# Optimization experiments

Hardware: AMD Instinct MI355X
Metric: run time of the kernel (lower is better)

## Reference

```python
import jax, jax.numpy as jnp
import numpy as np

EMBED_DIM = 128
NUM_HEADS = 4
HEAD_DIM = EMBED_DIM // NUM_HEADS


def setup_inputs() -> dict:
    key = jax.random.key(0)
    ks = jax.random.split(key, 12)
    B, N, D = 4, 4096, EMBED_DIM
    s = 1.0 / np.sqrt(D)
    inp = {
        "query": jax.random.normal(ks[0], (B, N, D), dtype=jnp.float32),
        "key": jax.random.normal(ks[1], (B, N, D), dtype=jnp.float32),
        "value": jax.random.normal(ks[2], (B, N, D), dtype=jnp.float32),
        "Wq": jax.random.uniform(ks[3], (D, D), jnp.float32, -s, s),
        "bq": jax.random.uniform(ks[4], (D,), jnp.float32, -s, s),
        "Wk": jax.random.uniform(ks[5], (D, D), jnp.float32, -s, s),
        "bk": jax.random.uniform(ks[6], (D,), jnp.float32, -s, s),
        "Wv": jax.random.uniform(ks[7], (D, D), jnp.float32, -s, s),
        "bv": jax.random.uniform(ks[8], (D,), jnp.float32, -s, s),
        "Wo": jax.random.uniform(ks[9], (D, D), jnp.float32, -s, s),
        "bo": jax.random.uniform(ks[10], (D,), jnp.float32, -s, s),
    }
    return inp


def reference(query, key, value, Wq, bq, Wk, bk, Wv, bv, Wo, bo):
    B, N, D = query.shape
    H, Dh = NUM_HEADS, HEAD_DIM
    scale = Dh ** -0.5
    # Linear projections (torch Linear: x @ W.T + b), split heads -> [B, H, N, Dh]
    Q = (query @ Wq.T + bq).reshape(B, N, H, Dh).transpose(0, 2, 1, 3)
    K = (key @ Wk.T + bk).reshape(B, N, H, Dh).transpose(0, 2, 1, 3)
    V = (value @ Wv.T + bv).reshape(B, N, H, Dh).transpose(0, 2, 1, 3)
    # Attention scores [B, H, N, N]
    scores = jnp.einsum('bhqd,bhkd->bhqk', Q, K) * scale
    attn = jax.nn.softmax(scores, axis=-1)
    ctx = jnp.einsum('bhqk,bhkd->bhqd', attn, V)  # [B, H, N, Dh]
    ctx = ctx.transpose(0, 2, 1, 3).reshape(B, N, D)
    return ctx @ Wo.T + bo
```

## Files before the change

### kernel.cpp

```cpp
#include <hip/hip_runtime.h>
#include <hip/hip_bf16.h>

#define N_SEQ 4096
#define DIM   128
#define NH    4
#define DH    32
#define BATCH 4

#define QSCALE 0.25503495870989204f

typedef __bf16 bf16x8 __attribute__((ext_vector_type(8)));
typedef __bf16 bf16x2 __attribute__((ext_vector_type(2)));
typedef __bf16 bf16x4 __attribute__((ext_vector_type(4)));
typedef float  f32x4  __attribute__((ext_vector_type(4)));

#define MFMA(a, b, c) __builtin_amdgcn_mfma_f32_16x16x32_bf16((a), (b), (c), 0, 0, 0)

static __device__ __forceinline__ bf16x8 cvt8(const float* __restrict__ p) {
    const float4* f4 = reinterpret_cast<const float4*>(p);
    float4 a = f4[0], b = f4[1];
    bf16x8 r;
    r[0] = (__bf16)a.x; r[1] = (__bf16)a.y; r[2] = (__bf16)a.z; r[3] = (__bf16)a.w;
    r[4] = (__bf16)b.x; r[5] = (__bf16)b.y; r[6] = (__bf16)b.z; r[7] = (__bf16)b.w;
    return r;
}

static __device__ __forceinline__ f32x4 exp4(f32x4 s) {
    f32x4 r;
    r[0] = __builtin_amdgcn_exp2f(s[0]);
    r[1] = __builtin_amdgcn_exp2f(s[1]);
    r[2] = __builtin_amdgcn_exp2f(s[2]);
    r[3] = __builtin_amdgcn_exp2f(s[3]);
    return r;
}

static __device__ __forceinline__ bf16x8 pack8(f32x4 a, f32x4 b) {
    bf16x8 o;
    o[0] = (__bf16)a[0]; o[1] = (__bf16)a[1];
    o[2] = (__bf16)a[2]; o[3] = (__bf16)a[3];
    o[4] = (__bf16)b[0]; o[5] = (__bf16)b[1];
    o[6] = (__bf16)b[2]; o[7] = (__bf16)b[3];
    return o;
}

__global__ __launch_bounds__(256) void proj_qkv(
    const float* __restrict__ xq, const float* __restrict__ xk, const float* __restrict__ xv,
    const float* __restrict__ Wq, const float* __restrict__ Wk, const float* __restrict__ Wv,
    const float* __restrict__ bq, const float* __restrict__ bk, const float* __restrict__ bv,
    __bf16* __restrict__ Qs, __bf16* __restrict__ Kb, __bf16* __restrict__ Vt)
{
    __shared__ __align__(16) char wlds[34816];
    const int z = blockIdx.z;
    const float* x    = (z == 0) ? xq : ((z == 1) ? xk : xv);
    const float* Wf   = (z == 0) ? Wq : ((z == 1) ? Wk : Wv);
    const float* bias = (z == 0) ? bq : ((z == 1) ? bk : bv);
    const int b    = blockIdx.y;
    const int tid  = threadIdx.x;
    const int wave = tid >> 6, lane = tid & 63;
    const int quad = lane >> 4, l15 = lane & 15;
    const int n0   = blockIdx.x * 64 + wave * 16;

    {
        const int r = tid >> 1, half = tid & 1;
        const float* wsrc = Wf + r * DIM + half * 64;
        char* wdst = wlds + r * 272 + half * 128;
        #pragma unroll
        for (int i = 0; i < 8; i++)
            *(bf16x8*)(wdst + i * 16) = cvt8(wsrc + i * 8);
    }

    bf16x8 a[4];
    const float* xrow = x + (b * N_SEQ + n0 + l15) * DIM + quad * 8;
    a[0] = cvt8(xrow);      a[1] = cvt8(xrow + 32);
    a[2] = cvt8(xrow + 64); a[3] = cvt8(xrow + 96);
    __syncthreads();

    const int n = n0 + l15;
    for (int t = 0; t < 8; t++) {
        const char* wr = wlds + (t * 16 + l15) * 272 + quad * 16;
        bf16x8 w0 = *(const bf16x8*)(wr);
        bf16x8 w1 = *(const bf16x8*)(wr + 64);
        bf16x8 w2 = *(const bf16x8*)(wr + 128);
        bf16x8 w3 = *(const bf16x8*)(wr + 192);

        f32x4 acc = {0.f, 0.f, 0.f, 0.f};
        acc = MFMA(w0, a[0], acc);
        acc = MFMA(w1, a[1], acc);
        acc = MFMA(w2, a[2], acc);
        acc = MFMA(w3, a[3], acc);

        const int d0 = t * 16 + quad * 4;
        if (z == 0) {
            const int h = d0 >> 5, dh0 = d0 & 31;
            bf16x4 q4;
            #pragma unroll
            for (int r = 0; r < 4; r++)
                q4[r] = (__bf16)((acc[r] + bias[d0 + r]) * QSCALE);
            *(bf16x4*)(Qs + ((b * NH + h) * N_SEQ + n) * DH + dh0) = q4;
        } else if (z == 1) {
            const int h = d0 >> 5, dh0 = d0 & 31;
            bf16x4 k4;
            #pragma unroll
            for (int r = 0; r < 4; r++)
                k4[r] = (__bf16)(acc[r] + bias[d0 + r]);
            *(bf16x4*)(Kb + ((b * NH + h) * N_SEQ + n) * DH + dh0) = k4;
        } else {
            const int nl = n & 63;
            const int np = (n & ~63) | (nl & 35) | ((nl & 12) << 1) | ((nl & 16) >> 2);
            #pragma unroll
            for (int r = 0; r < 4; r++) {
                const int d = d0 + r, h = d >> 5, dh = d & 31;
                Vt[((b * NH + h) * DH + dh) * N_SEQ + np] = (__bf16)(acc[r] + bias[d]);
            }
        }
    }
}

__global__ __launch_bounds__(256, 2) void flash_attn(
    const __bf16* __restrict__ Qs, const __bf16* __restrict__ Kb,
    const __bf16* __restrict__ Vt, __bf16* __restrict__ ctxb)
{
    __shared__ __align__(16) char smem[77824];
    char* const Kbase = smem;
    char* const Vbase = smem + 40960;

    const int bid  = blockIdx.x;
    const int bh   = bid & 15;
    const int qc   = bid >> 4;
    const int tid  = threadIdx.x;
    const int wave = tid >> 6, lane = tid & 63;
    const int quad = lane >> 4, l15 = lane & 15;
    const int qh   = wave & 1, kh = wave >> 1;
    const int n0   = qc * 128 + qh * 64;
    const int KH   = 2048;

    const __bf16* Qp = Qs + (bh * N_SEQ + n0) * DH;
    bf16x8 qf[4];
    #pragma unroll
    for (int q = 0; q < 4; q++)
        qf[q] = *(const bf16x8*)(Qp + (q * 16 + l15) * DH + quad * 8);

    bf16x8 ones;
    #pragma unroll
    for (int i = 0; i < 8; i++) ones[i] = (__bf16)1.0f;

    const int r_ = tid >> 2, c_ = tid & 3;
    const __bf16* gK = Kb + (size_t)bh * N_SEQ * DH + r_ * DH + c_ * 8;
    const __bf16* gV = Vt + ((size_t)bh * DH + (tid >> 3)) * N_SEQ + (tid & 7) * 8;
    const int kofsK = r_ * 80 + c_ * 16;
    const int kofsV = (tid >> 3) * 144 + (tid & 7) * 16;

    {
        #pragma unroll
        for (int g = 0; g < 2; g++) {
            #pragma unroll
            for (int t = 0; t < 2; t++) {
                bf16x8 kr = *(const bf16x8*)(gK + (size_t)(g * KH + t * 64) * DH);
                bf16x8 vr = *(const bf16x8*)(gV + g * KH + t * 64);
                *(bf16x8*)(Kbase + g * 20480 + t * 5120 + kofsK) = kr;
                *(bf16x8*)(Vbase + g * 18432 + t * 4608 + kofsV) = vr;
            }
        }
    }
    __syncthreads();

    char* const Kme = Kbase + kh * 20480;
    char* const Vme = Vbase + kh * 18432;

    f32x4 c[4][2];
    f32x4 cl[4];
    const f32x4 z4 = {0.f,0.f,0.f,0.f};
    #pragma unroll
    for (int q = 0; q < 4; q++) { c[q][0] = z4; c[q][1] = z4; cl[q] = z4; }

    for (int kbb = 0; kbb < KH / 128; kbb++) {
        const int cur = kbb & 1;
        const char* Kc = Kme + cur * 10240;
        const char* Vc = Vme + cur * 9216;

        const int kn = (kbb + 1) & (KH / 128 - 1);
        bf16x8 krn[2][2], vrn[2][2];
        #pragma unroll
        for (int g = 0; g < 2; g++) {
            #pragma unroll
            for (int t = 0; t < 2; t++) {
                krn[g][t] = *(const bf16x8*)(gK + (size_t)(g * KH + kn * 128 + t * 64) * DH);
                vrn[g][t] = *(const bf16x8*)(gV + g * KH + kn * 128 + t * 64);
            }
        }

        bf16x8 kfa[2][4], vfa[2][4];
        #pragma unroll
        for (int t = 0; t < 2; t++) {
            const char* Kt  = Kc + t * 5120;
            const char* Vtl = Vc + t * 4608;
            #pragma unroll
            for (int i = 0; i < 4; i++)
                kfa[t][i] = *(const bf16x8*)(Kt + (i * 16 + l15) * 80 + quad * 16);
            vfa[t][0] = *(const bf16x8*)(Vtl + l15 * 144 + quad * 16);
            vfa[t][1] = *(const bf16x8*)(Vtl + (16 + l15) * 144 + quad * 16);
            vfa[t][2] = *(const bf16x8*)(Vtl + l15 * 144 + 64 + quad * 16);
            vfa[t][3] = *(const bf16x8*)(Vtl + (16 + l15) * 144 + 64 + quad * 16);
        }

        #pragma unroll
        for (int t = 0; t < 2; t++) {
            bf16x8 pf[4][2];
            #pragma unroll
            for (int q = 0; q < 4; q++) {
                __builtin_amdgcn_s_setprio(1);
                f32x4 sa = MFMA(kfa[t][0], qf[q], z4);
                f32x4 sb = MFMA(kfa[t][1], qf[q], z4);
                f32x4 sc = MFMA(kfa[t][2], qf[q], z4);
                f32x4 sd = MFMA(kfa[t][3], qf[q], z4);
                __builtin_amdgcn_s_setprio(0);
                f32x4 ea = exp4(sa), eb = exp4(sb), ec = exp4(sc), ed = exp4(sd);
                pf[q][0] = pack8(ea, eb);
                pf[q][1] = pack8(ec, ed);
            }

            __builtin_amdgcn_s_setprio(1);
            #pragma unroll
            for (int q = 0; q < 4; q++) {
                c[q][0] = MFMA(vfa[t][0], pf[q][0], c[q][0]);
                c[q][1] = MFMA(vfa[t][1], pf[q][0], c[q][1]);
                c[q][0] = MFMA(vfa[t][2], pf[q][1], c[q][0]);
                c[q][1] = MFMA(vfa[t][3], pf[q][1], c[q][1]);
                cl[q]   = MFMA(ones, pf[q][0], cl[q]);
                cl[q]   = MFMA(ones, pf[q][1], cl[q]);
            }
            __builtin_amdgcn_s_setprio(0);
        }

        #pragma unroll
        for (int g = 0; g < 2; g++) {
            #pragma unroll
            for (int t = 0; t < 2; t++) {
                *(bf16x8*)(Kbase + g * 20480 + (cur ^ 1) * 10240 + t * 5120 + kofsK) = krn[g][t];
                *(bf16x8*)(Vbase + g * 18432 + (cur ^ 1) * 9216 + t * 4608 + kofsV) = vrn[g][t];
            }
        }
        __syncthreads();
    }


    if (kh == 1) {
        char* dst = smem + (qh * 64 + lane) * 144;
        #pragma unroll
        for (int q = 0; q < 4; q++) {
            *(f32x4*)(dst + (q * 2 + 0) * 16) = c[q][0];
            *(f32x4*)(dst + (q * 2 + 1) * 16) = c[q][1];
        }
        f32x4 lv = {cl[0][0], cl[1][0], cl[2][0], cl[3][0]};
        *(f32x4*)(dst + 128) = lv;
    }
    __syncthreads();
    if (kh == 0) {
        const char* src = smem + (qh * 64 + lane) * 144;
        f32x4 lp = *(const f32x4*)(src + 128);
        const int b = bh >> 2, h = bh & 3;
        #pragma unroll
        for (int q = 0; q < 4; q++) {
            c[q][0] += *(const f32x4*)(src + (q * 2 + 0) * 16);
            c[q][1] += *(const f32x4*)(src + (q * 2 + 1) * 16);
            const float inv = 1.0f / (cl[q][0] + lp[q]);
            const int qg = n0 + q * 16 + l15;
            __bf16* dst = ctxb + ((size_t)(b * N_SEQ + qg)) * DIM + h * DH + quad * 4;
            #pragma unroll
            for (int dt = 0; dt < 2; dt++) {
                f32x4 cc = c[q][dt];
                bf16x2 e0 = {(__bf16)(cc[0] * inv), (__bf16)(cc[1] * inv)};
                bf16x2 e1 = {(__bf16)(cc[2] * inv), (__bf16)(cc[3] * inv)};
                *(bf16x2*)(dst + dt * 16)     = e0;
                *(bf16x2*)(dst + dt * 16 + 2) = e1;
            }
        }
    }
}

__global__ __launch_bounds__(256) void out_proj(
    const __bf16* __restrict__ ctxb, const float* __restrict__ Wo,
    const float* __restrict__ bo, float* __restrict__ out)
{
    __shared__ __align__(16) char wlds[34816];
    const int b    = blockIdx.y;
    const int tid  = threadIdx.x;
    const int wave = tid >> 6, lane = tid & 63;
    const int quad = lane >> 4, l15 = lane & 15;
    const int n0   = blockIdx.x * 64 + wave * 16;

    {
        const int r = tid >> 1, half = tid & 1;
        const float* wsrc = Wo + r * DIM + half * 64;
        char* wdst = wlds + r * 272 + half * 128;
        #pragma unroll
        for (int i = 0; i < 8; i++)
            *(bf16x8*)(wdst + i * 16) = cvt8(wsrc + i * 8);
    }

    bf16x8 a[4];
    const __bf16* crow = ctxb + (b * N_SEQ + n0 + l15) * DIM + quad * 8;
    a[0] = *(const bf16x8*)(crow);
    a[1] = *(const bf16x8*)(crow + 32);
    a[2] = *(const bf16x8*)(crow + 64);
    a[3] = *(const bf16x8*)(crow + 96);
    __syncthreads();

    const int n = n0 + l15;
    for (int t = 0; t < 8; t++) {
        const char* wr = wlds + (t * 16 + l15) * 272 + quad * 16;
        bf16x8 w0 = *(const bf16x8*)(wr);
        bf16x8 w1 = *(const bf16x8*)(wr + 64);
        bf16x8 w2 = *(const bf16x8*)(wr + 128);
        bf16x8 w3 = *(const bf16x8*)(wr + 192);

        f32x4 acc = {0.f, 0.f, 0.f, 0.f};
        acc = MFMA(w0, a[0], acc);
        acc = MFMA(w1, a[1], acc);
        acc = MFMA(w2, a[2], acc);
        acc = MFMA(w3, a[3], acc);

        const int d0 = t * 16 + quad * 4;
        float4 o;
        o.x = acc[0] + bo[d0];
        o.y = acc[1] + bo[d0 + 1];
        o.z = acc[2] + bo[d0 + 2];
        o.w = acc[3] + bo[d0 + 3];
        *(float4*)(out + (b * N_SEQ + n) * DIM + d0) = o;
    }
}

extern "C" void kernel_launch(void* const* d_in, const int* in_sizes, int n_in,
                              void* d_out, int out_size, void* d_ws, size_t ws_size,
                              hipStream_t stream)
{
    const float* query = (const float*)d_in[0];
    const float* key   = (const float*)d_in[1];
    const float* value = (const float*)d_in[2];
    const float* Wq = (const float*)d_in[3];
    const float* bq = (const float*)d_in[4];
    const float* Wk = (const float*)d_in[5];
    const float* bk = (const float*)d_in[6];
    const float* Wv = (const float*)d_in[7];
    const float* bv = (const float*)d_in[8];
    const float* Wo = (const float*)d_in[9];
    const float* bo = (const float*)d_in[10];
    float* out = (float*)d_out;

    char* ws = (char*)d_ws;
    const size_t e = (size_t)BATCH * N_SEQ * DIM;
    __bf16* Qs   = (__bf16*)(ws);
    __bf16* Kb   = (__bf16*)(ws + 2 * e);
    __bf16* Vt   = (__bf16*)(ws + 4 * e);
    __bf16* ctxb = (__bf16*)(ws + 6 * e);

    proj_qkv<<<dim3(64, BATCH, 3), 256, 0, stream>>>(
        query, key, value, Wq, Wk, Wv, bq, bk, bv, Qs, Kb, Vt);
    flash_attn<<<dim3(512), 256, 0, stream>>>(Qs, Kb, Vt, ctxb);
    out_proj<<<dim3(64, BATCH), 256, 0, stream>>>(ctxb, Wo, bo, out);
}
```

Baseline: 147.4 us.

## Load K/V MFMA fragments directly from global into registers, dropping LDS staging

The flash attention loop no longer stages K and V tiles through double-buffered shared memory with a block-wide barrier each step. Each wave now loads its MFMA operand fragments straight from global memory into registers, using a two-register-set ping-pong prefetch. Shared memory shrinks to what the final cross-wave reduction needs. This removes LDS writes, LDS reads and __syncthreads per tile, which may allow higher occupancy. In exchange it gives up LDS reuse, so each wave issues its own strided global loads of K/V, which the L2 cache must absorb.

```diff
diff --git a/kernel.cpp b/kernel.cpp
--- a/kernel.cpp
+++ b/kernel.cpp
@@ -120,9 +120,7 @@
     const __bf16* __restrict__ Qs, const __bf16* __restrict__ Kb,
     const __bf16* __restrict__ Vt, __bf16* __restrict__ ctxb)
 {
-    __shared__ __align__(16) char smem[77824];
-    char* const Kbase = smem;
-    char* const Vbase = smem + 40960;
+    __shared__ __align__(16) char smem[18432];
 
     const int bid  = blockIdx.x;
     const int bh   = bid & 15;
@@ -144,28 +142,49 @@
     #pragma unroll
     for (int i = 0; i < 8; i++) ones[i] = (__bf16)1.0f;
 
-    const int r_ = tid >> 2, c_ = tid & 3;
-    const __bf16* gK = Kb + (size_t)bh * N_SEQ * DH + r_ * DH + c_ * 8;
-    const __bf16* gV = Vt + ((size_t)bh * DH + (tid >> 3)) * N_SEQ + (tid & 7) * 8;
-    const int kofsK = r_ * 80 + c_ * 16;
-    const int kofsV = (tid >> 3) * 144 + (tid & 7) * 16;
-
-    {
-        #pragma unroll
-        for (int g = 0; g < 2; g++) {
-            #pragma unroll
-            for (int t = 0; t < 2; t++) {
-                bf16x8 kr = *(const bf16x8*)(gK + (size_t)(g * KH + t * 64) * DH);
-                bf16x8 vr = *(const bf16x8*)(gV + g * KH + t * 64);
-                *(bf16x8*)(Kbase + g * 20480 + t * 5120 + kofsK) = kr;
-                *(bf16x8*)(Vbase + g * 18432 + t * 4608 + kofsV) = vr;
-            }
-        }
-    }
-    __syncthreads();
-
-    char* const Kme = Kbase + kh * 20480;
-    char* const Vme = Vbase + kh * 18432;
+    const __bf16* gK  = Kb + ((size_t)bh * N_SEQ + kh * KH + l15) * DH + quad * 8;
+    const __bf16* gV0 = Vt + ((size_t)bh * DH + l15) * N_SEQ + kh * KH + quad * 8;
+    const __bf16* gV1 = gV0 + 16 * N_SEQ;
+
+#define LOADT(t, k0,k1,k2,k3, v0,v1,v2,v3) do {                         \
+    const int _t = (t) & 31;                                            \
+    const __bf16* _k = gK + (size_t)(_t * 64) * DH;                     \
+    k0 = *(const bf16x8*)(_k);                                          \
+    k1 = *(const bf16x8*)(_k + 16 * DH);                                \
+    k2 = *(const bf16x8*)(_k + 32 * DH);                                \
+    k3 = *(const bf16x8*)(_k + 48 * DH);                                \
+    v0 = *(const bf16x8*)(gV0 + _t * 64);                               \
+    v1 = *(const bf16x8*)(gV1 + _t * 64);                               \
+    v2 = *(const bf16x8*)(gV0 + _t * 64 + 32);                          \
+    v3 = *(const bf16x8*)(gV1 + _t * 64 + 32);                          \
+} while (0)
+
+#define COMPUTE(k0,k1,k2,k3, v0,v1,v2,v3) do {                          \
+    bf16x8 pf[4][2];                                                    \
+    _Pragma("unroll")                                                   \
+    for (int q = 0; q < 4; q++) {                                       \
+        __builtin_amdgcn_s_setprio(1);                                  \
+        f32x4 sa = MFMA(k0, qf[q], z4);                                 \
+        f32x4 sb = MFMA(k1, qf[q], z4);                                 \
+        f32x4 sc = MFMA(k2, qf[q], z4);                                 \
+        f32x4 sd = MFMA(k3, qf[q], z4);                                 \
+        __builtin_amdgcn_s_setprio(0);                                  \
+        f32x4 ea = exp4(sa), eb = exp4(sb), ec = exp4(sc), ed = exp4(sd); \
+        pf[q][0] = pack8(ea, eb);                                       \
+        pf[q][1] = pack8(ec, ed);                                       \
+    }                                                                   \
+    __builtin_amdgcn_s_setprio(1);                                      \
+    _Pragma("unroll")                                                   \
+    for (int q = 0; q < 4; q++) {                                       \
+        c[q][0] = MFMA(v0, pf[q][0], c[q][0]);                          \
+        c[q][1] = MFMA(v1, pf[q][0], c[q][1]);                          \
+        c[q][0] = MFMA(v2, pf[q][1], c[q][0]);                          \
+        c[q][1] = MFMA(v3, pf[q][1], c[q][1]);                          \
+        cl[q]   = MFMA(ones, pf[q][0], cl[q]);                          \
+        cl[q]   = MFMA(ones, pf[q][1], cl[q]);                          \
+    }                                                                   \
+    __builtin_amdgcn_s_setprio(0);                                      \
+} while (0)
 
     f32x4 c[4][2];
     f32x4 cl[4];
@@ -173,76 +192,20 @@
     #pragma unroll
     for (int q = 0; q < 4; q++) { c[q][0] = z4; c[q][1] = z4; cl[q] = z4; }
 
-    for (int kbb = 0; kbb < KH / 128; kbb++) {
-        const int cur = kbb & 1;
-        const char* Kc = Kme + cur * 10240;
-        const char* Vc = Vme + cur * 9216;
-
-        const int kn = (kbb + 1) & (KH / 128 - 1);
-        bf16x8 krn[2][2], vrn[2][2];
-        #pragma unroll
-        for (int g = 0; g < 2; g++) {
-            #pragma unroll
-            for (int t = 0; t < 2; t++) {
-                krn[g][t] = *(const bf16x8*)(gK + (size_t)(g * KH + kn * 128 + t * 64) * DH);
-                vrn[g][t] = *(const bf16x8*)(gV + g * KH + kn * 128 + t * 64);
-            }
-        }
-
-        bf16x8 kfa[2][4], vfa[2][4];
-        #pragma unroll
-        for (int t = 0; t < 2; t++) {
-            const char* Kt  = Kc + t * 5120;
-            const char* Vtl = Vc + t * 4608;
-            #pragma unroll
-            for (int i = 0; i < 4; i++)
-                kfa[t][i] = *(const bf16x8*)(Kt + (i * 16 + l15) * 80 + quad * 16);
-            vfa[t][0] = *(const bf16x8*)(Vtl + l15 * 144 + quad * 16);
-            vfa[t][1] = *(const bf16x8*)(Vtl + (16 + l15) * 144 + quad * 16);
-            vfa[t][2] = *(const bf16x8*)(Vtl + l15 * 144 + 64 + quad * 16);
-            vfa[t][3] = *(const bf16x8*)(Vtl + (16 + l15) * 144 + 64 + quad * 16);
-        }
-
-        #pragma unroll
-        for (int t = 0; t < 2; t++) {
-            bf16x8 pf[4][2];
-            #pragma unroll
-            for (int q = 0; q < 4; q++) {
-                __builtin_amdgcn_s_setprio(1);
-                f32x4 sa = MFMA(kfa[t][0], qf[q], z4);
-                f32x4 sb = MFMA(kfa[t][1], qf[q], z4);
-                f32x4 sc = MFMA(kfa[t][2], qf[q], z4);
-                f32x4 sd = MFMA(kfa[t][3], qf[q], z4);
-                __builtin_amdgcn_s_setprio(0);
-                f32x4 ea = exp4(sa), eb = exp4(sb), ec = exp4(sc), ed = exp4(sd);
-                pf[q][0] = pack8(ea, eb);
-                pf[q][1] = pack8(ec, ed);
-            }
-
-            __builtin_amdgcn_s_setprio(1);
-            #pragma unroll
-            for (int q = 0; q < 4; q++) {
-                c[q][0] = MFMA(vfa[t][0], pf[q][0], c[q][0]);
-                c[q][1] = MFMA(vfa[t][1], pf[q][0], c[q][1]);
-                c[q][0] = MFMA(vfa[t][2], pf[q][1], c[q][0]);
-                c[q][1] = MFMA(vfa[t][3], pf[q][1], c[q][1]);
-                cl[q]   = MFMA(ones, pf[q][0], cl[q]);
-                cl[q]   = MFMA(ones, pf[q][1], cl[q]);
-            }
-            __builtin_amdgcn_s_setprio(0);
-        }
-
-        #pragma unroll
-        for (int g = 0; g < 2; g++) {
-            #pragma unroll
-            for (int t = 0; t < 2; t++) {
-                *(bf16x8*)(Kbase + g * 20480 + (cur ^ 1) * 10240 + t * 5120 + kofsK) = krn[g][t];
-                *(bf16x8*)(Vbase + g * 18432 + (cur ^ 1) * 9216 + t * 4608 + kofsV) = vrn[g][t];
-            }
-        }
-        __syncthreads();
-    }
-
+    bf16x8 kA0,kA1,kA2,kA3, vA0,vA1,vA2,vA3;
+    bf16x8 kB0,kB1,kB2,kB3, vB0,vB1,vB2,vB3;
+
+    LOADT(0, kA0,kA1,kA2,kA3, vA0,vA1,vA2,vA3);
+
+    for (int t = 0; t < 32; t += 2) {
+        LOADT(t + 1, kB0,kB1,kB2,kB3, vB0,vB1,vB2,vB3);
+        COMPUTE(kA0,kA1,kA2,kA3, vA0,vA1,vA2,vA3);
+        LOADT(t + 2, kA0,kA1,kA2,kA3, vA0,vA1,vA2,vA3);
+        COMPUTE(kB0,kB1,kB2,kB3, vB0,vB1,vB2,vB3);
+    }
+
+#undef LOADT
+#undef COMPUTE
 
     if (kh == 1) {
         char* dst = smem + (qh * 64 + lane) * 144;
```

New measurement: 151.8 us. +3.0%, slower.
